# Kernel tuning notes

Measured on AMD Instinct MI355X. Metric: run time of the kernel, lower is better.

The kernel has to match this reference:

```python
import jax, jax.numpy as jnp
import numpy as np

S = 2   # upsample scale
K = 5   # reassembly kernel k_up


def setup_inputs() -> dict:
    key = jax.random.key(0)
    ks = jax.random.split(key, 7)
    B, C, H, W = 4, 128, 64, 64
    C_MID = 64
    return {
        "x": jax.random.normal(ks[0], (B, C, H, W), dtype=jnp.float32),
        "w1": jax.random.normal(ks[1], (C_MID, C), dtype=jnp.float32) * 0.05,
        "w2": jax.random.normal(ks[2], (S * S * K * K, C_MID, 3, 3), dtype=jnp.float32) * 0.05,
        "bn_gamma": jax.random.uniform(ks[3], (C_MID,), dtype=jnp.float32, minval=0.5, maxval=1.5),
        "bn_beta": jax.random.normal(ks[4], (C_MID,), dtype=jnp.float32) * 0.1,
        "bn_mean": jax.random.normal(ks[5], (C_MID,), dtype=jnp.float32) * 0.1,
        "bn_var": jax.random.uniform(ks[6], (C_MID,), dtype=jnp.float32, minval=0.5, maxval=1.5),
    }


def reference(x, w1, w2, bn_gamma, bn_beta, bn_mean, bn_var):
    B, C, H, W = x.shape
    s, k = S, K
    eps = 1e-5
    # --- content encoder: 1x1 conv -> BN (inference form) -> ReLU -> 3x3 conv ---
    h = jnp.einsum('bchw,oc->bohw', x, w1)  # (B, c_mid, H, W)
    inv = bn_gamma / jnp.sqrt(bn_var + eps)
    h = h * inv[None, :, None, None] + (bn_beta - bn_mean * inv)[None, :, None, None]
    h = jax.nn.relu(h)
    ker = jax.lax.conv_general_dilated(
        h, w2, window_strides=(1, 1), padding=((1, 1), (1, 1)),
        dimension_numbers=('NCHW', 'OIHW', 'NCHW'))  # (B, s*s*k*k, H, W)
    # softmax over the k*k reassembly window
    ker = jax.nn.softmax(ker.reshape(B, s * s, k * k, H, W), axis=2)
    # --- unfold k x k neighborhoods of x (row-major window order, as F.unfold) ---
    p = k // 2
    xp = jnp.pad(x, ((0, 0), (0, 0), (p, p), (p, p)))
    patches = jnp.stack(
        [xp[:, :, i:i + H, j:j + W] for i in range(k) for j in range(k)],
        axis=2)  # (B, C, k*k, H, W)
    # weighted reassembly: sum over the k*k window per (sub-pixel, channel)
    out = jnp.einsum('bckhw,bskhw->bcshw', patches, ker)  # (B, C, s*s, H, W)
    # pixel shuffle: (B, C, s, s, H, W) -> (B, C, H*s, W*s)
    out = out.reshape(B, C, s, s, H, W).transpose(0, 1, 4, 2, 5, 3)
    return out.reshape(B, C, H * s, W * s)
```

## Files before the change

kernel.cpp:

```cpp
#include <hip/hip_runtime.h>
#include <hip/hip_bf16.h>

#define HW 4096

typedef __attribute__((ext_vector_type(8))) short  short8;
typedef __attribute__((ext_vector_type(4))) float  floatx4;
typedef __attribute__((ext_vector_type(4))) unsigned short ushort4v;

#define OFF_W2B 0ul
#define OFF_W1B 129024ul
#define OFF_BN  145408ul
#define OFF_XG  145920ul
#define OFF_XPP 4340224ul

__global__ __launch_bounds__(256) void prep_kernel(const float* __restrict__ x,
                                                   const float* __restrict__ w1,
                                                   const float* __restrict__ w2,
                                                   const float* __restrict__ gamma,
                                                   const float* __restrict__ beta,
                                                   const float* __restrict__ mean,
                                                   const float* __restrict__ var,
                                                   char* __restrict__ ws) {
    int tid = blockIdx.x * 256 + threadIdx.x;
    if (tid < 262144) {
        int pix = tid & 4095;
        int cq  = (tid >> 12) & 15;
        int b   = tid >> 16;
        const float* xp = x + ((size_t)(b * 128 + cq * 8)) * HW + pix;
        union { short8 s; __hip_bfloat16 h[8]; } u;
        #pragma unroll
        for (int cc = 0; cc < 8; ++cc) u.h[cc] = __float2bfloat16(xp[(size_t)cc * HW]);
        *(short8*)((__hip_bfloat16*)(ws + OFF_XG) + (size_t)tid * 8) = u.s;
        return;
    }
    int t2 = tid - 262144;
    if (t2 < 64512) {
        int n = t2 / 576;
        int k = t2 - n * 576;
        int t = k >> 6, c = k & 63;
        float v = (n < 100) ? w2[(n * 64 + c) * 9 + t] : 0.f;
        ((__hip_bfloat16*)(ws + OFF_W2B))[t2] = __float2bfloat16(v);
    } else if (t2 < 64512 + 8192) {
        int i = t2 - 64512;
        ((__hip_bfloat16*)(ws + OFF_W1B))[i] = __float2bfloat16(w1[i]);
    } else if (t2 < 64512 + 8192 + 64) {
        int o = t2 - 64512 - 8192;
        float inv = gamma[o] * rsqrtf(var[o] + 1e-5f);
        ((float2*)(ws + OFF_BN))[o] = make_float2(inv, beta[o] - mean[o] * inv);
    } else {
        int t3 = t2 - 72768;
        if (t3 < 591872) {
            int j  = t3 % 17;
            int rr = t3 / 17;
            int row68 = rr - (rr / 68) * 68;
            int bc = rr / 68;
            int gy = row68 - 2;
            const float* xp = x + (size_t)bc * HW + (size_t)gy * 64;
            union { ushort4v u4; __hip_bfloat16 h[4]; } u;
            #pragma unroll
            for (int e = 0; e < 4; ++e) {
                int gx = j * 4 + e - 2;
                float f = 0.f;
                if ((unsigned)gy < 64u && (unsigned)gx < 64u) f = xp[gx];
                u.h[e] = __float2bfloat16(f);
            }
            *(ushort4v*)((__hip_bfloat16*)(ws + OFF_XPP) + (size_t)rr * 68 + j * 4) = u.u4;
        }
    }
}

__global__ __launch_bounds__(512, 8) void fused_carafe(const char* __restrict__ ws,
                                                       float* __restrict__ out) {
    __shared__ __align__(16) char smem[40064];
    __hip_bfloat16* xsT = (__hip_bfloat16*)smem;
    float*          lg  = (float*)(smem + 16384);
    __hip_bfloat16* hs  = (__hip_bfloat16*)(smem + 23680);
    __hip_bfloat16* Whi = (__hip_bfloat16*)(smem + 23680);

    int b    = blockIdx.x >> 8;
    int tile = blockIdx.x & 255;
    int ty0 = (tile >> 4) * 4;
    int tx0 = (tile & 15) * 4;
    int tid = threadIdx.x;
    int lane = tid & 63, wave = tid >> 6;
    int q = lane >> 4, m = lane & 15;

    const __hip_bfloat16* xpp = (const __hip_bfloat16*)(ws + OFF_XPP);
    #pragma unroll
    for (int it = 0; it < 2; ++it) {
        int idx = tid + it * 512;
        int c = idx >> 3, h = idx & 7;
        size_t rb = ((size_t)(b * 128 + c) * 68 + (ty0 + h)) * 68 + tx0;
        union { short8 s; uint2 d[2]; } u;
        u.d[0] = *(const uint2*)(xpp + rb);
        u.d[1] = *(const uint2*)(xpp + rb + 4);
        *(short8*)(xsT + c * 64 + ((h ^ (c & 7)) << 3)) = u.s;
    }

    {
        const __hip_bfloat16* xg  = (const __hip_bfloat16*)(ws + OFF_XG) + (size_t)b * 16 * 4096 * 8;
        const __hip_bfloat16* w1b = (const __hip_bfloat16*)(ws + OFF_W1B);
        for (int task = wave; task < 12; task += 8) {
            int mt = task >> 2, nt = task & 3;
            int bo = nt * 16 + m;
            float2 bnia = ((const float2*)(ws + OFF_BN))[bo];
            int hp = mt * 16 + m;
            int hpc = (hp < 36) ? hp : 0;
            int hy1 = hpc / 6, hx1 = hpc - hy1 * 6;
            int gy = ty0 + hy1 - 1, gx = tx0 + hx1 - 1;
            int gyc = min(max(gy, 0), 63), gxc = min(max(gx, 0), 63);
            int pix = gyc * 64 + gxc;
            floatx4 acc;
            #pragma unroll
            for (int r = 0; r < 4; ++r) acc[r] = 0.f;
            #pragma unroll
            for (int s = 0; s < 4; ++s) {
                short8 a  = *(const short8*)(xg + ((size_t)((s * 4 + q) * 4096 + pix)) * 8);
                short8 bw = *(const short8*)(w1b + bo * 128 + s * 32 + q * 8);
                acc = __builtin_amdgcn_mfma_f32_16x16x32_bf16(a, bw, acc, 0, 0, 0);
            }
            #pragma unroll
            for (int r = 0; r < 4; ++r) {
                int prow = mt * 16 + q * 4 + r;
                if (prow < 36) {
                    int phy = prow / 6, phx = prow - phy * 6;
                    int gy2 = ty0 + phy - 1, gx2 = tx0 + phx - 1;
                    bool in = ((unsigned)gy2 < 64u) && ((unsigned)gx2 < 64u);
                    float v = in ? fmaxf(fmaf(acc[r], bnia.x, bnia.y), 0.f) : 0.f;
                    hs[prow * 64 + ((((bo >> 3) ^ (prow & 7)) << 3) | (bo & 7))] = __float2bfloat16(v);
                }
            }
        }
    }
    __syncthreads();

    if (wave < 7) {
        int nt = wave;
        int py = m >> 2, px = m & 3;
        const __hip_bfloat16* w2b = (const __hip_bfloat16*)(ws + OFF_W2B);
        const __hip_bfloat16* bp  = w2b + (size_t)(nt * 16 + m) * 576 + q * 8;

        floatx4 acc;
        #pragma unroll
        for (int r = 0; r < 4; ++r) acc[r] = 0.f;

        short8 bcur = *(const short8*)bp;
        for (int s = 0; s < 18; ++s) {
            int t = s >> 1, co = (s & 1) * 4 + q;
            int ti = t / 3, tj = t - ti * 3;
            int row = (py + ti) * 6 + (px + tj);
            short8 a = *(const short8*)(hs + row * 64 + ((co ^ (row & 7)) << 3));
            short8 bn2 = bcur;
            if (s < 17) bn2 = *(const short8*)(bp + (s + 1) * 32);
            acc = __builtin_amdgcn_mfma_f32_16x16x32_bf16(a, bcur, acc, 0, 0, 0);
            bcur = bn2;
        }
        #pragma unroll
        for (int r = 0; r < 4; ++r)
            lg[(q * 4 + r) * 114 + nt * 16 + m] = acc[r];
    }
    __syncthreads();

    {
        short8 z;
        #pragma unroll
        for (int j = 0; j < 8; ++j) z[j] = 0;
        *(short8*)((char*)Whi + tid * 16) = z;
        *(short8*)((char*)Whi + 8192 + tid * 16) = z;
    }
    __syncthreads();

    if (tid < 64) {
        int pixid = tid >> 2, g = tid & 3;
        int py = pixid >> 2, px = pixid & 3;
        float v[25];
        #pragma unroll
        for (int wi = 0; wi < 25; ++wi) v[wi] = lg[pixid * 114 + g * 25 + wi];
        float mx = v[0];
        #pragma unroll
        for (int wi = 1; wi < 25; ++wi) mx = fmaxf(mx, v[wi]);
        float ssum = 0.f;
        #pragma unroll
        for (int wi = 0; wi < 25; ++wi) { v[wi] = __expf(v[wi] - mx); ssum += v[wi]; }
        float rs = 1.f / ssum;
        int row = tid;
        #pragma unroll
        for (int t25 = 0; t25 < 25; ++t25) {
            int ti = t25 / 5, tj = t25 - ti * 5;
            int addr = row * 64 + ((((py + ti) ^ (row & 7)) << 3) | (px + tj));
            float kv = v[t25] * rs;
            __hip_bfloat16 khi = __float2bfloat16(kv);
            Whi[addr] = khi;
            Whi[4096 + addr] = __float2bfloat16(kv - __bfloat162float(khi));
        }
    }
    __syncthreads();

    {
        int nt = wave;
        int c = nt * 16 + m;
        const __hip_bfloat16* xr = xsT + c * 64;
        short8 b0 = *(const short8*)(xr + ((q ^ (c & 7)) << 3));
        short8 b1 = *(const short8*)(xr + (((4 + q) ^ (c & 7)) << 3));
        float* outc = out + (((size_t)b * 128 + c) << 14);
        #pragma unroll
        for (int mt = 0; mt < 4; ++mt) {
            int row = mt * 16 + m;
            const __hip_bfloat16* wr = Whi + row * 64;
            int s0 = ((q ^ (row & 7)) << 3);
            int s1 = (((4 + q) ^ (row & 7)) << 3);
            short8 ah0 = *(const short8*)(wr + s0);
            short8 al0 = *(const short8*)(wr + 4096 + s0);
            short8 ah1 = *(const short8*)(wr + s1);
            short8 al1 = *(const short8*)(wr + 4096 + s1);
            floatx4 acc;
            #pragma unroll
            for (int r = 0; r < 4; ++r) acc[r] = 0.f;
            acc = __builtin_amdgcn_mfma_f32_16x16x32_bf16(ah0, b0, acc, 0, 0, 0);
            acc = __builtin_amdgcn_mfma_f32_16x16x32_bf16(al0, b0, acc, 0, 0, 0);
            acc = __builtin_amdgcn_mfma_f32_16x16x32_bf16(ah1, b1, acc, 0, 0, 0);
            acc = __builtin_amdgcn_mfma_f32_16x16x32_bf16(al1, b1, acc, 0, 0, 0);
            float* op = outc + (size_t)(2 * (ty0 + mt)) * 128 + 2 * (tx0 + q);
            *(float2*)op         = make_float2(acc[0], acc[1]);
            *(float2*)(op + 128) = make_float2(acc[2], acc[3]);
        }
    }
}

extern "C" void kernel_launch(void* const* d_in, const int* in_sizes, int n_in,
                              void* d_out, int out_size, void* d_ws, size_t ws_size,
                              hipStream_t stream) {
    const float* x     = (const float*)d_in[0];
    const float* w1    = (const float*)d_in[1];
    const float* w2    = (const float*)d_in[2];
    const float* gamma = (const float*)d_in[3];
    const float* beta  = (const float*)d_in[4];
    const float* mean  = (const float*)d_in[5];
    const float* var   = (const float*)d_in[6];
    float* out = (float*)d_out;
    char*  ws  = (char*)d_ws;

    prep_kernel<<<3621, 256, 0, stream>>>(x, w1, w2, gamma, beta, mean, var, ws);
    fused_carafe<<<1024, 512, 0, stream>>>(ws, out);
}
```

Measured before the change: 118.4 us.

## Split fused CARAFE kernel into separate 1x1 GEMM, 3x3 conv, and reassembly kernels

New measurement: 131.2 us. 10.8% more time.

```diff
diff --git a/kernel.cpp b/kernel.cpp
--- a/kernel.cpp
+++ b/kernel.cpp
@@ -12,6 +12,12 @@
 #define OFF_BN  145408ul
 #define OFF_XG  145920ul
 #define OFF_XPP 4340224ul
+#define OFF_HT  9075200ul
+#define OFF_KER 11172352ul
+
+__device__ __forceinline__ float bfbits(unsigned u) {
+    union { unsigned u; float f; } t; t.u = u; return t.f;
+}
 
 __global__ __launch_bounds__(256) void prep_kernel(const float* __restrict__ x,
                                                    const float* __restrict__ w1,
@@ -69,13 +75,131 @@
     }
 }
 
-__global__ __launch_bounds__(512, 8) void fused_carafe(const char* __restrict__ ws,
-                                                       float* __restrict__ out) {
-    __shared__ __align__(16) char smem[40064];
+__global__ __launch_bounds__(256) void k1_hgemm(const char* __restrict__ ws,
+                                               char* __restrict__ wso) {
+    __shared__ __align__(16) __hip_bfloat16 hb[64 * 72];
+    int b = blockIdx.x >> 6;
+    int blockpix = (blockIdx.x & 63) * 64;
+    int tid = threadIdx.x;
+    int lane = tid & 63, wave = tid >> 6;
+    int q = lane >> 4, m = lane & 15;
+
+    const __hip_bfloat16* xg  = (const __hip_bfloat16*)(ws + OFF_XG) + (size_t)b * 16 * 4096 * 8;
+    const __hip_bfloat16* w1b = (const __hip_bfloat16*)(ws + OFF_W1B);
+    int pix = blockpix + wave * 16 + m;
+
+    #pragma unroll
+    for (int nt = 0; nt < 4; ++nt) {
+        int bo = nt * 16 + m;
+        float2 bnia = ((const float2*)(ws + OFF_BN))[bo];
+        floatx4 acc;
+        #pragma unroll
+        for (int r = 0; r < 4; ++r) acc[r] = 0.f;
+        #pragma unroll
+        for (int s = 0; s < 4; ++s) {
+            short8 a  = *(const short8*)(xg + ((size_t)((s * 4 + q) * 4096 + pix)) * 8);
+            short8 bw = *(const short8*)(w1b + bo * 128 + s * 32 + q * 8);
+            acc = __builtin_amdgcn_mfma_f32_16x16x32_bf16(a, bw, acc, 0, 0, 0);
+        }
+        #pragma unroll
+        for (int r = 0; r < 4; ++r) {
+            float v = fmaxf(fmaf(acc[r], bnia.x, bnia.y), 0.f);
+            hb[(wave * 16 + q * 4 + r) * 72 + bo] = __float2bfloat16(v);
+        }
+    }
+    __syncthreads();
+
+    __hip_bfloat16* ht = (__hip_bfloat16*)(wso + OFF_HT);
+    int lrow = tid >> 2, e0 = (tid & 3) * 16;
+    __hip_bfloat16* dst = ht + ((size_t)b * 4096 + blockpix + lrow) * 64 + e0;
+    *(short8*)(dst)     = *(const short8*)(&hb[lrow * 72 + e0]);
+    *(short8*)(dst + 8) = *(const short8*)(&hb[lrow * 72 + e0 + 8]);
+}
+
+__global__ __launch_bounds__(256) void k2_conv(const char* __restrict__ ws,
+                                               char* __restrict__ wso) {
+    __shared__ __align__(16) char smem[41984];
+    __hip_bfloat16* hs = (__hip_bfloat16*)smem;
+    float*          lg = (float*)(smem + 12800);
+
+    int b = blockIdx.x >> 6;
+    int t = blockIdx.x & 63;
+    int ty0 = (t >> 3) * 8, tx0 = (t & 7) * 8;
+    int tid = threadIdx.x;
+    int lane = tid & 63, wave = tid >> 6;
+    int q = lane >> 4, m = lane & 15;
+
+    const __hip_bfloat16* ht = (const __hip_bfloat16*)(ws + OFF_HT);
+    #pragma unroll
+    for (int it = 0; it < 4; ++it) {
+        int idx = it * 256 + tid;
+        if (idx < 800) {
+            int row = idx >> 3, co = idx & 7;
+            int hy = row / 10, hx = row - hy * 10;
+            int gy = ty0 + hy - 1, gx = tx0 + hx - 1;
+            short8 v;
+            #pragma unroll
+            for (int j = 0; j < 8; ++j) v[j] = 0;
+            if ((unsigned)gy < 64u && (unsigned)gx < 64u)
+                v = *(const short8*)(ht + ((size_t)b * 4096 + gy * 64 + gx) * 64 + co * 8);
+            *(short8*)(&hs[row * 64 + ((co ^ (row & 7)) << 3)]) = v;
+        }
+    }
+    __syncthreads();
+
+    {
+        int mt = wave;
+        int pixidx = mt * 16 + m;
+        int py = pixidx >> 3, px = pixidx & 7;
+        const __hip_bfloat16* w2b = (const __hip_bfloat16*)(ws + OFF_W2B);
+        for (int nt = 0; nt < 7; ++nt) {
+            const __hip_bfloat16* bp = w2b + (size_t)(nt * 16 + m) * 576 + q * 8;
+            floatx4 acc;
+            #pragma unroll
+            for (int r = 0; r < 4; ++r) acc[r] = 0.f;
+            short8 bcur = *(const short8*)bp;
+            for (int s = 0; s < 18; ++s) {
+                int tt = s >> 1, co = (s & 1) * 4 + q;
+                int ti = tt / 3, tj = tt - ti * 3;
+                int row = (py + ti) * 10 + (px + tj);
+                short8 a = *(const short8*)(&hs[row * 64 + ((co ^ (row & 7)) << 3)]);
+                short8 bn2 = bcur;
+                if (s < 17) bn2 = *(const short8*)(bp + (s + 1) * 32);
+                acc = __builtin_amdgcn_mfma_f32_16x16x32_bf16(a, bcur, acc, 0, 0, 0);
+                bcur = bn2;
+            }
+            #pragma unroll
+            for (int r = 0; r < 4; ++r)
+                lg[(mt * 16 + q * 4 + r) * 114 + nt * 16 + m] = acc[r];
+        }
+    }
+    __syncthreads();
+
+    {
+        int pixloc = tid & 63, g = tid >> 6;
+        float v[25];
+        #pragma unroll
+        for (int wi = 0; wi < 25; ++wi) v[wi] = lg[pixloc * 114 + g * 25 + wi];
+        float mx = v[0];
+        #pragma unroll
+        for (int wi = 1; wi < 25; ++wi) mx = fmaxf(mx, v[wi]);
+        float ssum = 0.f;
+        #pragma unroll
+        for (int wi = 0; wi < 25; ++wi) { v[wi] = __expf(v[wi] - mx); ssum += v[wi]; }
+        float rs = 1.f / ssum;
+        int gpix = (ty0 + (pixloc >> 3)) * 64 + tx0 + (pixloc & 7);
+        float* ker = (float*)(wso + OFF_KER);
+        #pragma unroll
+        for (int t25 = 0; t25 < 25; ++t25)
+            ker[(((size_t)(b * 4 + g) * 25 + t25)) * 4096 + gpix] = v[t25] * rs;
+    }
+}
+
+__global__ __launch_bounds__(256) void k3_reassemble(const char* __restrict__ ws,
+                                                     float* __restrict__ out) {
+    __shared__ __align__(16) char smem[32768];
     __hip_bfloat16* xsT = (__hip_bfloat16*)smem;
-    float*          lg  = (float*)(smem + 16384);
-    __hip_bfloat16* hs  = (__hip_bfloat16*)(smem + 23680);
-    __hip_bfloat16* Whi = (__hip_bfloat16*)(smem + 23680);
+    __hip_bfloat16* Whi = (__hip_bfloat16*)(smem + 16384);
 
     int b    = blockIdx.x >> 8;
     int tile = blockIdx.x & 255;
@@ -87,8 +211,8 @@
 
     const __hip_bfloat16* xpp = (const __hip_bfloat16*)(ws + OFF_XPP);
     #pragma unroll
-    for (int it = 0; it < 2; ++it) {
-        int idx = tid + it * 512;
+    for (int it = 0; it < 4; ++it) {
+        int idx = it * 256 + tid;
         int c = idx >> 3, h = idx & 7;
         size_t rb = ((size_t)(b * 128 + c) * 68 + (ty0 + h)) * 68 + tx0;
         union { short8 s; uint2 d[2]; } u;
@@ -96,99 +220,38 @@
         u.d[1] = *(const uint2*)(xpp + rb + 4);
         *(short8*)(xsT + c * 64 + ((h ^ (c & 7)) << 3)) = u.s;
     }
-
-    {
-        const __hip_bfloat16* xg  = (const __hip_bfloat16*)(ws + OFF_XG) + (size_t)b * 16 * 4096 * 8;
-        const __hip_bfloat16* w1b = (const __hip_bfloat16*)(ws + OFF_W1B);
-        for (int task = wave; task < 12; task += 8) {
-            int mt = task >> 2, nt = task & 3;
-            int bo = nt * 16 + m;
-            float2 bnia = ((const float2*)(ws + OFF_BN))[bo];
-            int hp = mt * 16 + m;
-            int hpc = (hp < 36) ? hp : 0;
-            int hy1 = hpc / 6, hx1 = hpc - hy1 * 6;
-            int gy = ty0 + hy1 - 1, gx = tx0 + hx1 - 1;
-            int gyc = min(max(gy, 0), 63), gxc = min(max(gx, 0), 63);
-            int pix = gyc * 64 + gxc;
-            floatx4 acc;
-            #pragma unroll
-            for (int r = 0; r < 4; ++r) acc[r] = 0.f;
-            #pragma unroll
-            for (int s = 0; s < 4; ++s) {
-                short8 a  = *(const short8*)(xg + ((size_t)((s * 4 + q) * 4096 + pix)) * 8);
-                short8 bw = *(const short8*)(w1b + bo * 128 + s * 32 + q * 8);
-                acc = __builtin_amdgcn_mfma_f32_16x16x32_bf16(a, bw, acc, 0, 0, 0);
-            }
-            #pragma unroll
-            for (int r = 0; r < 4; ++r) {
-                int prow = mt * 16 + q * 4 + r;
-                if (prow < 36) {
-                    int phy = prow / 6, phx = prow - phy * 6;
-                    int gy2 = ty0 + phy - 1, gx2 = tx0 + phx - 1;
-                    bool in = ((unsigned)gy2 < 64u) && ((unsigned)gx2 < 64u);
-                    float v = in ? fmaxf(fmaf(acc[r], bnia.x, bnia.y), 0.f) : 0.f;
-                    hs[prow * 64 + ((((bo >> 3) ^ (prow & 7)) << 3) | (bo & 7))] = __float2bfloat16(v);
-                }
-            }
-        }
-    }
-    __syncthreads();
-
-    if (wave < 7) {
-        int nt = wave;
-        int py = m >> 2, px = m & 3;
-        const __hip_bfloat16* w2b = (const __hip_bfloat16*)(ws + OFF_W2B);
-        const __hip_bfloat16* bp  = w2b + (size_t)(nt * 16 + m) * 576 + q * 8;
-
-        floatx4 acc;
-        #pragma unroll
-        for (int r = 0; r < 4; ++r) acc[r] = 0.f;
-
-        short8 bcur = *(const short8*)bp;
-        for (int s = 0; s < 18; ++s) {
-            int t = s >> 1, co = (s & 1) * 4 + q;
-            int ti = t / 3, tj = t - ti * 3;
-            int row = (py + ti) * 6 + (px + tj);
-            short8 a = *(const short8*)(hs + row * 64 + ((co ^ (row & 7)) << 3));
-            short8 bn2 = bcur;
-            if (s < 17) bn2 = *(const short8*)(bp + (s + 1) * 32);
-            acc = __builtin_amdgcn_mfma_f32_16x16x32_bf16(a, bcur, acc, 0, 0, 0);
-            bcur = bn2;
-        }
-        #pragma unroll
-        for (int r = 0; r < 4; ++r)
-            lg[(q * 4 + r) * 114 + nt * 16 + m] = acc[r];
-    }
-    __syncthreads();
-
     {
         short8 z;
         #pragma unroll
         for (int j = 0; j < 8; ++j) z[j] = 0;
-        *(short8*)((char*)Whi + tid * 16) = z;
-        *(short8*)((char*)Whi + 8192 + tid * 16) = z;
-    }
-    __syncthreads();
-
-    if (tid < 64) {
-        int pixid = tid >> 2, g = tid & 3;
+        char* wb = (char*)Whi + tid * 64;
+        #pragma unroll
+        for (int j = 0; j < 4; ++j) *(short8*)(wb + j * 16) = z;
+    }
+    __syncthreads();
+
+    short8 eb[2][2];
+    int ecs[2];
+    #pragma unroll
+    for (int ntl = 0; ntl < 2; ++ntl) {
+        int c = (wave * 2 + ntl) * 16 + m;
+        ecs[ntl] = c;
+        const __hip_bfloat16* xr = xsT + c * 64;
+        eb[ntl][0] = *(const short8*)(xr + ((q ^ (c & 7)) << 3));
+        eb[ntl][1] = *(const short8*)(xr + (((4 + q) ^ (c & 7)) << 3));
+    }
+
+    {
+        const float* ker = (const float*)(ws + OFF_KER);
+        int row = tid >> 2, tq = tid & 2 ? (tid & 3) : (tid & 3);
+        tq = tid & 3;
+        int pixid = row >> 2, g = row & 3;
         int py = pixid >> 2, px = pixid & 3;
-        float v[25];
-        #pragma unroll
-        for (int wi = 0; wi < 25; ++wi) v[wi] = lg[pixid * 114 + g * 25 + wi];
-        float mx = v[0];
-        #pragma unroll
-        for (int wi = 1; wi < 25; ++wi) mx = fmaxf(mx, v[wi]);
-        float ssum = 0.f;
-        #pragma unroll
-        for (int wi = 0; wi < 25; ++wi) { v[wi] = __expf(v[wi] - mx); ssum += v[wi]; }
-        float rs = 1.f / ssum;
-        int row = tid;
-        #pragma unroll
-        for (int t25 = 0; t25 < 25; ++t25) {
+        int gpix = (ty0 + py) * 64 + (tx0 + px);
+        for (int t25 = tq; t25 < 25; t25 += 4) {
+            float kv = ker[(((size_t)(b * 4 + g) * 25 + t25)) * 4096 + gpix];
             int ti = t25 / 5, tj = t25 - ti * 5;
             int addr = row * 64 + ((((py + ti) ^ (row & 7)) << 3) | (px + tj));
-            float kv = v[t25] * rs;
             __hip_bfloat16 khi = __float2bfloat16(kv);
             Whi[addr] = khi;
             Whi[4096 + addr] = __float2bfloat16(kv - __bfloat162float(khi));
@@ -196,31 +259,27 @@
     }
     __syncthreads();
 
-    {
-        int nt = wave;
-        int c = nt * 16 + m;
-        const __hip_bfloat16* xr = xsT + c * 64;
-        short8 b0 = *(const short8*)(xr + ((q ^ (c & 7)) << 3));
-        short8 b1 = *(const short8*)(xr + (((4 + q) ^ (c & 7)) << 3));
-        float* outc = out + (((size_t)b * 128 + c) << 14);
-        #pragma unroll
-        for (int mt = 0; mt < 4; ++mt) {
-            int row = mt * 16 + m;
-            const __hip_bfloat16* wr = Whi + row * 64;
-            int s0 = ((q ^ (row & 7)) << 3);
-            int s1 = (((4 + q) ^ (row & 7)) << 3);
-            short8 ah0 = *(const short8*)(wr + s0);
-            short8 al0 = *(const short8*)(wr + 4096 + s0);
-            short8 ah1 = *(const short8*)(wr + s1);
-            short8 al1 = *(const short8*)(wr + 4096 + s1);
+    #pragma unroll
+    for (int mt = 0; mt < 4; ++mt) {
+        int row = mt * 16 + m;
+        const __hip_bfloat16* wr = Whi + row * 64;
+        int s0 = ((q ^ (row & 7)) << 3);
+        int s1 = (((4 + q) ^ (row & 7)) << 3);
+        short8 ah0 = *(const short8*)(wr + s0);
+        short8 al0 = *(const short8*)(wr + 4096 + s0);
+        short8 ah1 = *(const short8*)(wr + s1);
+        short8 al1 = *(const short8*)(wr + 4096 + s1);
+        #pragma unroll
+        for (int ntl = 0; ntl < 2; ++ntl) {
             floatx4 acc;
             #pragma unroll
             for (int r = 0; r < 4; ++r) acc[r] = 0.f;
-            acc = __builtin_amdgcn_mfma_f32_16x16x32_bf16(ah0, b0, acc, 0, 0, 0);
-            acc = __builtin_amdgcn_mfma_f32_16x16x32_bf16(al0, b0, acc, 0, 0, 0);
-            acc = __builtin_amdgcn_mfma_f32_16x16x32_bf16(ah1, b1, acc, 0, 0, 0);
-            acc = __builtin_amdgcn_mfma_f32_16x16x32_bf16(al1, b1, acc, 0, 0, 0);
-            float* op = outc + (size_t)(2 * (ty0 + mt)) * 128 + 2 * (tx0 + q);
+            acc = __builtin_amdgcn_mfma_f32_16x16x32_bf16(ah0, eb[ntl][0], acc, 0, 0, 0);
+            acc = __builtin_amdgcn_mfma_f32_16x16x32_bf16(al0, eb[ntl][0], acc, 0, 0, 0);
+            acc = __builtin_amdgcn_mfma_f32_16x16x32_bf16(ah1, eb[ntl][1], acc, 0, 0, 0);
+            acc = __builtin_amdgcn_mfma_f32_16x16x32_bf16(al1, eb[ntl][1], acc, 0, 0, 0);
+            float* op = out + (((size_t)b * 128 + ecs[ntl]) << 14)
+                      + (size_t)(2 * (ty0 + mt)) * 128 + 2 * (tx0 + q);
             *(float2*)op         = make_float2(acc[0], acc[1]);
             *(float2*)(op + 128) = make_float2(acc[2], acc[3]);
         }
@@ -241,5 +300,7 @@
     char*  ws  = (char*)d_ws;
 
     prep_kernel<<<3621, 256, 0, stream>>>(x, w1, w2, gamma, beta, mean, var, ws);
-    fused_carafe<<<1024, 512, 0, stream>>>(ws, out);
-}
+    k1_hgemm<<<256, 256, 0, stream>>>(ws, ws);
+    k2_conv<<<256, 256, 0, stream>>>(ws, ws);
+    k3_reassemble<<<1024, 256, 0, stream>>>(ws, out);
+}
```

## Parallelize softmax across all threads and transpose reassembly MFMA operand roles

Applied to the files above, without the earlier changes.

Measured after the change: 116.3 us. No clear change (-1.7%).

```diff
diff --git a/kernel.cpp b/kernel.cpp
--- a/kernel.cpp
+++ b/kernel.cpp
@@ -69,7 +69,7 @@
     }
 }
 
-__global__ __launch_bounds__(512, 8) void fused_carafe(const char* __restrict__ ws,
+__global__ __launch_bounds__(512, 4) void fused_carafe(const char* __restrict__ ws,
                                                        float* __restrict__ out) {
     __shared__ __align__(16) char smem[40064];
     __hip_bfloat16* xsT = (__hip_bfloat16*)smem;
@@ -170,59 +170,74 @@
     }
     __syncthreads();
 
-    if (tid < 64) {
-        int pixid = tid >> 2, g = tid & 3;
+    {
+        int row = tid >> 3;
+        int sub = tid & 7;
+        int pixid = row >> 2, g = row & 3;
         int py = pixid >> 2, px = pixid & 3;
-        float v[25];
-        #pragma unroll
-        for (int wi = 0; wi < 25; ++wi) v[wi] = lg[pixid * 114 + g * 25 + wi];
-        float mx = v[0];
-        #pragma unroll
-        for (int wi = 1; wi < 25; ++wi) mx = fmaxf(mx, v[wi]);
+        float v[4];
+        float mx = -1e30f;
+        #pragma unroll
+        for (int k = 0; k < 4; ++k) {
+            int t25 = sub + k * 8;
+            v[k] = (t25 < 25) ? lg[pixid * 114 + g * 25 + t25] : -1e30f;
+            mx = fmaxf(mx, v[k]);
+        }
+        #pragma unroll
+        for (int d = 1; d < 8; d <<= 1) mx = fmaxf(mx, __shfl_xor(mx, d, 64));
         float ssum = 0.f;
         #pragma unroll
-        for (int wi = 0; wi < 25; ++wi) { v[wi] = __expf(v[wi] - mx); ssum += v[wi]; }
+        for (int k = 0; k < 4; ++k) { v[k] = __expf(v[k] - mx); ssum += v[k]; }
+        #pragma unroll
+        for (int d = 1; d < 8; d <<= 1) ssum += __shfl_xor(ssum, d, 64);
         float rs = 1.f / ssum;
-        int row = tid;
-        #pragma unroll
-        for (int t25 = 0; t25 < 25; ++t25) {
-            int ti = t25 / 5, tj = t25 - ti * 5;
-            int addr = row * 64 + ((((py + ti) ^ (row & 7)) << 3) | (px + tj));
-            float kv = v[t25] * rs;
-            __hip_bfloat16 khi = __float2bfloat16(kv);
-            Whi[addr] = khi;
-            Whi[4096 + addr] = __float2bfloat16(kv - __bfloat162float(khi));
-        }
-    }
-    __syncthreads();
-
-    {
-        int nt = wave;
-        int c = nt * 16 + m;
-        const __hip_bfloat16* xr = xsT + c * 64;
-        short8 b0 = *(const short8*)(xr + ((q ^ (c & 7)) << 3));
-        short8 b1 = *(const short8*)(xr + (((4 + q) ^ (c & 7)) << 3));
-        float* outc = out + (((size_t)b * 128 + c) << 14);
-        #pragma unroll
-        for (int mt = 0; mt < 4; ++mt) {
-            int row = mt * 16 + m;
-            const __hip_bfloat16* wr = Whi + row * 64;
-            int s0 = ((q ^ (row & 7)) << 3);
-            int s1 = (((4 + q) ^ (row & 7)) << 3);
-            short8 ah0 = *(const short8*)(wr + s0);
-            short8 al0 = *(const short8*)(wr + 4096 + s0);
-            short8 ah1 = *(const short8*)(wr + s1);
-            short8 al1 = *(const short8*)(wr + 4096 + s1);
+        #pragma unroll
+        for (int k = 0; k < 4; ++k) {
+            int t25 = sub + k * 8;
+            if (t25 < 25) {
+                int ti = t25 / 5, tj = t25 - ti * 5;
+                int addr = row * 64 + ((((py + ti) ^ (row & 7)) << 3) | (px + tj));
+                float kv = v[k] * rs;
+                __hip_bfloat16 khi = __float2bfloat16(kv);
+                Whi[addr] = khi;
+                Whi[4096 + addr] = __float2bfloat16(kv - __bfloat162float(khi));
+            }
+        }
+    }
+    __syncthreads();
+
+    {
+        int pt = wave & 3, ch = wave >> 2;
+        int browW = pt * 16 + m;
+        const __hip_bfloat16* wr = Whi + browW * 64;
+        int s0 = ((q ^ (browW & 7)) << 3);
+        int s1 = (((4 + q) ^ (browW & 7)) << 3);
+        short8 bh0 = *(const short8*)(wr + s0);
+        short8 bl0 = *(const short8*)(wr + 4096 + s0);
+        short8 bh1 = *(const short8*)(wr + s1);
+        short8 bl1 = *(const short8*)(wr + 4096 + s1);
+
+        int px = m >> 2;
+        int gy = (m >> 1) & 1, gx = m & 1;
+        size_t rowoff = (size_t)(2 * (ty0 + pt) + gy) * 128 + 2 * (tx0 + px) + gx;
+
+        #pragma unroll
+        for (int ct = 0; ct < 4; ++ct) {
+            int ca = ch * 64 + ct * 16 + m;
+            const __hip_bfloat16* xr = xsT + ca * 64;
+            short8 a0 = *(const short8*)(xr + ((q ^ (ca & 7)) << 3));
+            short8 a1 = *(const short8*)(xr + (((4 + q) ^ (ca & 7)) << 3));
             floatx4 acc;
             #pragma unroll
             for (int r = 0; r < 4; ++r) acc[r] = 0.f;
-            acc = __builtin_amdgcn_mfma_f32_16x16x32_bf16(ah0, b0, acc, 0, 0, 0);
-            acc = __builtin_amdgcn_mfma_f32_16x16x32_bf16(al0, b0, acc, 0, 0, 0);
-            acc = __builtin_amdgcn_mfma_f32_16x16x32_bf16(ah1, b1, acc, 0, 0, 0);
-            acc = __builtin_amdgcn_mfma_f32_16x16x32_bf16(al1, b1, acc, 0, 0, 0);
-            float* op = outc + (size_t)(2 * (ty0 + mt)) * 128 + 2 * (tx0 + q);
-            *(float2*)op         = make_float2(acc[0], acc[1]);
-            *(float2*)(op + 128) = make_float2(acc[2], acc[3]);
+            acc = __builtin_amdgcn_mfma_f32_16x16x32_bf16(a0, bh0, acc, 0, 0, 0);
+            acc = __builtin_amdgcn_mfma_f32_16x16x32_bf16(a0, bl0, acc, 0, 0, 0);
+            acc = __builtin_amdgcn_mfma_f32_16x16x32_bf16(a1, bh1, acc, 0, 0, 0);
+            acc = __builtin_amdgcn_mfma_f32_16x16x32_bf16(a1, bl1, acc, 0, 0, 0);
+            int cbase = ch * 64 + ct * 16 + q * 4;
+            #pragma unroll
+            for (int r = 0; r < 4; ++r)
+                out[(((size_t)(b * 128 + cbase + r)) << 14) + rowoff] = acc[r];
         }
     }
 }
```
